# Kernel optimization log

Measured on AMD Instinct MI355X. Metric: run time of the kernel, lower is better.

## Reference

```python
import jax, jax.numpy as jnp
import numpy as np

N, F_IN, H, F_OUT, E = 50000, 128, 8, 16, 800000


def setup_inputs() -> dict:
    key = jax.random.key(0)
    ks = jax.random.split(key, 10)
    x = jax.random.normal(ks[0], (N, F_IN), dtype=jnp.float32)
    edge_index = jax.random.randint(ks[1], (2, E), 0, N, dtype=jnp.int64 if jax.config.read('jax_enable_x64') else jnp.int32)
    edge_prob = jax.random.uniform(ks[2], (E, 1), dtype=jnp.float32)
    s = 1.0 / np.sqrt(F_IN)
    Wp = jax.random.normal(ks[3], (H * F_OUT, F_IN), dtype=jnp.float32) * s
    Wt = jax.random.normal(ks[4], (H * F_OUT, 1), dtype=jnp.float32)
    a_src = jax.random.normal(ks[5], (H, F_OUT), dtype=jnp.float32) * 0.1
    a_trg = jax.random.normal(ks[6], (H, F_OUT), dtype=jnp.float32) * 0.1
    a_tp = jax.random.normal(ks[7], (H, F_OUT), dtype=jnp.float32) * 0.1
    Wskip = jax.random.normal(ks[8], (H * F_OUT, F_IN), dtype=jnp.float32) * s
    bias = jnp.zeros((H * F_OUT,), dtype=jnp.float32)
    return {"x": x, "edge_index": edge_index, "edge_prob": edge_prob,
            "Wp": Wp, "Wt": Wt, "a_src": a_src, "a_trg": a_trg,
            "a_tp": a_tp, "Wskip": Wskip, "bias": bias}


def reference(x, edge_index, edge_prob, Wp, Wt, a_src, a_trg, a_tp, Wskip, bias):
    n = x.shape[0]
    h, f = a_src.shape
    src, trg = edge_index[0], edge_index[1]
    # node projection: [N, H, F_out]
    proj = (x @ Wp.T).reshape(n, h, f)
    # transition-prob projection: [E, H, F_out]
    trans = (edge_prob @ Wt.T).reshape(-1, h, f)
    # per-node source/target scores [N, H], per-edge prob score [E, H]
    s_src = jnp.einsum('nhf,hf->nh', proj, a_src)
    s_trg = jnp.einsum('nhf,hf->nh', proj, a_trg)
    s_tp = jnp.einsum('ehf,hf->eh', trans, a_tp)
    scores = jax.nn.leaky_relu(s_src[src] + s_trg[trg] + s_tp, negative_slope=0.2)
    # global-max-shifted exp, segment softmax over target nodes
    e = jnp.exp(scores - jnp.max(scores))
    denom = jax.ops.segment_sum(e, trg, num_segments=n)
    attn = e / (denom[trg] + 1e-16)  # [E, H]
    weighted = proj[src] * attn[..., None]  # [E, H, F_out]
    out = jax.ops.segment_sum(weighted, trg, num_segments=n)  # [N, H, F_out]
    # skip connection (F_out != F_in -> skip_proj path), concat heads, bias, ELU
    out = out + (x @ Wskip.T).reshape(n, h, f)
    out = out.reshape(n, h * f) + bias
    return jax.nn.elu(out)
```

## Files before the change

### kernel.cpp

```cpp
#include <hip/hip_runtime.h>
#include <hip/hip_fp16.h>
#include <math.h>

constexpr int Nn  = 50000;
constexpr int FIN = 128;
constexpr int NH  = 8;
constexpr int FO  = 16;
constexpr int HF  = 128;
constexpr int NWR = 272;
constexpr int NPREP = NWR / 2;
constexpr int NBLK64 = (Nn + 63) / 64;
constexpr int NSCAN = (Nn + 255) / 256;

typedef _Float16 f16x8 __attribute__((ext_vector_type(8)));
typedef float    f32x4 __attribute__((ext_vector_type(4)));

__global__ __launch_bounds__(256) void k_pc(
    const float* __restrict__ Wp, const float* __restrict__ Wskip,
    const float* __restrict__ a_src, const float* __restrict__ a_trg,
    const float* __restrict__ Wt, const float* __restrict__ a_tp,
    _Float16* __restrict__ Wh, float* __restrict__ ctp,
    const int* __restrict__ trg, int* __restrict__ deg,
    int* __restrict__ rank, int E)
{
    const int bid = blockIdx.x;
    if (bid < NPREP) {
        if (bid == 0 && threadIdx.x < NH) {
            int h = threadIdx.x;
            float s = 0.f;
            #pragma unroll
            for (int f = 0; f < FO; ++f) s += Wt[h * FO + f] * a_tp[h * FO + f];
            ctp[h] = s;
        }
        const int o = bid * 2 + (threadIdx.x >> 7);
        const int k = threadIdx.x & 127;
        float v;
        if (o < 128)      v = Wp[o * FIN + k];
        else if (o < 256) v = Wskip[(o - 128) * FIN + k];
        else if (o < 264) {
            const int h = o - 256;
            float s = 0.f;
            #pragma unroll
            for (int f = 0; f < FO; ++f)
                s += a_src[h * FO + f] * Wp[(h * FO + f) * FIN + k];
            v = s;
        } else {
            const int h = o - 264;
            float s = 0.f;
            #pragma unroll
            for (int f = 0; f < FO; ++f)
                s += a_trg[h * FO + f] * Wp[(h * FO + f) * FIN + k];
            v = s;
        }
        Wh[o * FIN + k] = (_Float16)v;
        return;
    }

    int e = (bid - NPREP) * 256 + threadIdx.x;
    if (e < E) rank[e] = atomicAdd(&deg[trg[e]], 1);
}

__global__ __launch_bounds__(256) void k_scan1(const int* __restrict__ deg,
                                               int* __restrict__ partial)
{
    __shared__ int lds[256];
    int t = threadIdx.x, i = blockIdx.x * 256 + t;
    lds[t] = (i < Nn) ? deg[i] : 0;
    __syncthreads();
    for (int off = 128; off > 0; off >>= 1) {
        if (t < off) lds[t] += lds[t + off];
        __syncthreads();
    }
    if (t == 0) partial[blockIdx.x] = lds[0];
}

__global__ __launch_bounds__(256) void k_scan3(const int* __restrict__ deg,
                                               const int* __restrict__ partial,
                                               int* __restrict__ pos)
{
    __shared__ int lds[256], lds2[256];
    const int t = threadIdx.x;
    const int i = blockIdx.x * 256 + t;
    lds2[t] = (t < NSCAN) ? partial[t] : 0;
    __syncthreads();
    for (int off = 1; off < 256; off <<= 1) {
        int u = (t >= off) ? lds2[t - off] : 0;
        __syncthreads();
        lds2[t] += u;
        __syncthreads();
    }
    const int base = (blockIdx.x == 0) ? 0 : lds2[blockIdx.x - 1];
    int v = (i < Nn) ? deg[i] : 0;
    lds[t] = v;
    __syncthreads();
    for (int off = 1; off < 256; off <<= 1) {
        int u = (t >= off) ? lds[t - off] : 0;
        __syncthreads();
        lds[t] += u;
        __syncthreads();
    }
    if (i < Nn) pos[i] = base + lds[t] - v;
}

__global__ __launch_bounds__(256) void k_fn(
    const int* __restrict__ src, const int* __restrict__ trg,
    const float* __restrict__ prob, const int* __restrict__ rank,
    const int* __restrict__ pos, unsigned int* __restrict__ spk,
    const float* __restrict__ x, const _Float16* __restrict__ Wh,
    const float* __restrict__ bias,
    __half* __restrict__ projA, float* __restrict__ out,
    float* __restrict__ ssrc, float* __restrict__ strg_s, int E, int nbFill)
{
    const int bid = blockIdx.x;

    if (bid < nbFill) {
        int e4 = bid * 256 + threadIdx.x;
        if (e4 * 4 < E) {
            int4   s4 = reinterpret_cast<const int4*>(src)[e4];
            int4   t4 = reinterpret_cast<const int4*>(trg)[e4];
            float4 p4 = reinterpret_cast<const float4*>(prob)[e4];
            int4   r4 = reinterpret_cast<const int4*>(rank)[e4];
            int    sv[4] = {s4.x, s4.y, s4.z, s4.w};
            int    tv[4] = {t4.x, t4.y, t4.z, t4.w};
            int    rv[4] = {r4.x, r4.y, r4.z, r4.w};
            float  pv[4] = {p4.x, p4.y, p4.z, p4.w};
            #pragma unroll
            for (int i = 0; i < 4; ++i) {
                int slot = pos[tv[i]] + rv[i];
                spk[slot] = (unsigned int)sv[i] |
                    ((unsigned int)__half_as_ushort(__float2half_rn(pv[i])) << 16);
            }
        }
        return;
    }

    const int g0 = (bid - nbFill) * 64;
    const int w  = threadIdx.x >> 6;
    const int l  = threadIdx.x & 63;
    const int lr = l & 15;
    const int kb = l >> 4;
    const int t0 = w * 4;

    f16x8 b[4][4];
    const _Float16* wb = Wh + (size_t)lr * FIN + kb * 8;
    #pragma unroll
    for (int i = 0; i < 4; ++i) {
        #pragma unroll
        for (int ks = 0; ks < 4; ++ks)
            b[i][ks] = *reinterpret_cast<const f16x8*>(
                wb + (size_t)(t0 + i) * 16 * FIN + ks * 32);
    }
    f16x8 b16[4];
    if (w == 3) {
        #pragma unroll
        for (int ks = 0; ks < 4; ++ks)
            b16[ks] = *reinterpret_cast<const f16x8*>(
                wb + (size_t)16 * 16 * FIN + ks * 32);
    }

    const float* xr0 = x + (size_t)(g0 + lr) * FIN + kb * 8;

    if (g0 + 64 <= Nn) {
        float4 ucur[8];
        #pragma unroll
        for (int q = 0; q < 8; ++q)
            ucur[q] = *reinterpret_cast<const float4*>(
                xr0 + (q >> 1) * 32 + (q & 1) * 4);

        #pragma unroll
        for (int ng = 0; ng < 4; ++ng) {
            float4 unx[8];
            if (ng < 3) {
                const float* xrn = xr0 + (size_t)(ng + 1) * 16 * FIN;
                #pragma unroll
                for (int q = 0; q < 8; ++q)
                    unx[q] = *reinterpret_cast<const float4*>(
                        xrn + (q >> 1) * 32 + (q & 1) * 4);
            }

            f16x8 a[4];
            #pragma unroll
            for (int ks = 0; ks < 4; ++ks) {
                float4 lo = ucur[ks * 2], hi = ucur[ks * 2 + 1];
                a[ks][0] = (_Float16)lo.x; a[ks][1] = (_Float16)lo.y;
                a[ks][2] = (_Float16)lo.z; a[ks][3] = (_Float16)lo.w;
                a[ks][4] = (_Float16)hi.x; a[ks][5] = (_Float16)hi.y;
                a[ks][6] = (_Float16)hi.z; a[ks][7] = (_Float16)hi.w;
            }

            f32x4 acc[4];
            #pragma unroll
            for (int i = 0; i < 4; ++i) acc[i] = (f32x4){0.f, 0.f, 0.f, 0.f};
            f32x4 acc16 = (f32x4){0.f, 0.f, 0.f, 0.f};

            #pragma unroll
            for (int i = 0; i < 4; ++i) {
                #pragma unroll
                for (int ks = 0; ks < 4; ++ks)
                    acc[i] = __builtin_amdgcn_mfma_f32_16x16x32_f16(
                        a[ks], b[i][ks], acc[i], 0, 0, 0);
            }
            if (w == 3) {
                #pragma unroll
                for (int ks = 0; ks < 4; ++ks)
                    acc16 = __builtin_amdgcn_mfma_f32_16x16x32_f16(
                        a[ks], b16[ks], acc16, 0, 0, 0);
            }

            const int n0 = g0 + ng * 16;
            #pragma unroll
            for (int r = 0; r < 4; ++r) {
                const int n = n0 + kb * 4 + r;
                if (t0 < 8) {
                    #pragma unroll
                    for (int i = 0; i < 4; ++i)
                        projA[(size_t)n * HF + (t0 + i) * FO + lr] =
                            __float2half_rn(acc[i][r]);
                } else {
                    #pragma unroll
                    for (int i = 0; i < 4; ++i) {
                        const int o = (t0 + i - 8) * 16 + lr;
                        out[(size_t)n * HF + o] = acc[i][r] + bias[o];
                    }
                }
                if (w == 3) {
                    if (lr < 8) ssrc[n * 8 + lr] = acc16[r];
                    else        strg_s[n * 8 + (lr - 8)] = acc16[r];
                }
            }

            #pragma unroll
            for (int q = 0; q < 8; ++q) ucur[q] = unx[q];
        }
    } else {
        f16x8 a[4];
        #pragma unroll
        for (int ks = 0; ks < 4; ++ks) {
            float4 u0 = *reinterpret_cast<const float4*>(xr0 + ks * 32);
            float4 u1 = *reinterpret_cast<const float4*>(xr0 + ks * 32 + 4);
            a[ks][0] = (_Float16)u0.x; a[ks][1] = (_Float16)u0.y;
            a[ks][2] = (_Float16)u0.z; a[ks][3] = (_Float16)u0.w;
            a[ks][4] = (_Float16)u1.x; a[ks][5] = (_Float16)u1.y;
            a[ks][6] = (_Float16)u1.z; a[ks][7] = (_Float16)u1.w;
        }

        f32x4 acc[4];
        #pragma unroll
        for (int i = 0; i < 4; ++i) acc[i] = (f32x4){0.f, 0.f, 0.f, 0.f};
        f32x4 acc16 = (f32x4){0.f, 0.f, 0.f, 0.f};

        #pragma unroll
        for (int i = 0; i < 4; ++i) {
            #pragma unroll
            for (int ks = 0; ks < 4; ++ks)
                acc[i] = __builtin_amdgcn_mfma_f32_16x16x32_f16(
                    a[ks], b[i][ks], acc[i], 0, 0, 0);
        }
        if (w == 3) {
            #pragma unroll
            for (int ks = 0; ks < 4; ++ks)
                acc16 = __builtin_amdgcn_mfma_f32_16x16x32_f16(
                    a[ks], b16[ks], acc16, 0, 0, 0);
        }

        #pragma unroll
        for (int r = 0; r < 4; ++r) {
            const int n = g0 + kb * 4 + r;
            if (t0 < 8) {
                #pragma unroll
                for (int i = 0; i < 4; ++i)
                    projA[(size_t)n * HF + (t0 + i) * FO + lr] =
                        __float2half_rn(acc[i][r]);
            } else {
                #pragma unroll
                for (int i = 0; i < 4; ++i) {
                    const int o = (t0 + i - 8) * 16 + lr;
                    out[(size_t)n * HF + o] = acc[i][r] + bias[o];
                }
            }
            if (w == 3) {
                if (lr < 8) ssrc[n * 8 + lr] = acc16[r];
                else        strg_s[n * 8 + (lr - 8)] = acc16[r];
            }
        }
    }
}

__global__ __launch_bounds__(256) void k_gather(
    const unsigned int* __restrict__ spk, const int* __restrict__ pos,
    const float* __restrict__ ssrc, const float* __restrict__ strg_s,
    const float* __restrict__ ctp,
    const __half2* __restrict__ projA, float* __restrict__ out, int E)
{
    const int wv   = threadIdx.x >> 6;
    const int n    = blockIdx.x * 4 + wv;
    const int lane = threadIdx.x & 63;
    const int h    = lane >> 3;
    const int f2   = lane & 7;

    const int jb = pos[n];
    const int je = (n + 1 < Nn) ? pos[n + 1] : E;
    const float st  = strg_s[n * 8 + h];
    const float cth = ctp[h];
    const float* __restrict__ ssl = ssrc + h;
    const __half2* __restrict__ pA = projA + h * 8 + f2;

    float num0 = 0.f, num1 = 0.f, den = 0.f;
    int j = jb;
    for (; j + 3 < je; j += 4) {
        const unsigned int pk0 = spk[j];
        const unsigned int pk1 = spk[j + 1];
        const unsigned int pk2 = spk[j + 2];
        const unsigned int pk3 = spk[j + 3];
        const int s0 = pk0 & 0xFFFF, s1 = pk1 & 0xFFFF;
        const int s2 = pk2 & 0xFFFF, s3 = pk3 & 0xFFFF;
        const float ss0 = ssl[s0 * 8], ss1 = ssl[s1 * 8];
        const float ss2 = ssl[s2 * 8], ss3 = ssl[s3 * 8];
        const __half2 g0 = pA[s0 * 64], g1 = pA[s1 * 64];
        const __half2 g2 = pA[s2 * 64], g3 = pA[s3 * 64];
        const float p0 = __half2float(__ushort_as_half((unsigned short)(pk0 >> 16)));
        const float p1 = __half2float(__ushort_as_half((unsigned short)(pk1 >> 16)));
        const float p2 = __half2float(__ushort_as_half((unsigned short)(pk2 >> 16)));
        const float p3 = __half2float(__ushort_as_half((unsigned short)(pk3 >> 16)));
        float sc0 = ss0 + st + cth * p0;
        float sc1 = ss1 + st + cth * p1;
        float sc2 = ss2 + st + cth * p2;
        float sc3 = ss3 + st + cth * p3;
        sc0 = fmaxf(sc0, 0.2f * sc0);
        sc1 = fmaxf(sc1, 0.2f * sc1);
        sc2 = fmaxf(sc2, 0.2f * sc2);
        sc3 = fmaxf(sc3, 0.2f * sc3);
        const float ev0 = __expf(sc0), ev1 = __expf(sc1);
        const float ev2 = __expf(sc2), ev3 = __expf(sc3);
        const float2 G0 = __half22float2(g0), G1 = __half22float2(g1);
        const float2 G2 = __half22float2(g2), G3 = __half22float2(g3);
        den  += (ev0 + ev1) + (ev2 + ev3);
        num0 += ev0 * G0.x + ev1 * G1.x + ev2 * G2.x + ev3 * G3.x;
        num1 += ev0 * G0.y + ev1 * G1.y + ev2 * G2.y + ev3 * G3.y;
    }
    for (; j < je; ++j) {
        const unsigned int pk = spk[j];
        const int s = pk & 0xFFFF;
        const float p = __half2float(__ushort_as_half((unsigned short)(pk >> 16)));
        float sc = ssl[s * 8] + st + cth * p;
        sc = fmaxf(sc, 0.2f * sc);
        const float ev = __expf(sc);
        const float2 G = __half22float2(pA[s * 64]);
        den  += ev;
        num0 += ev * G.x;
        num1 += ev * G.y;
    }

    const float inv = 1.f / (den + 1e-16f);
    const int idx = n * HF + h * FO + f2 * 2;
    float2 o = *reinterpret_cast<const float2*>(&out[idx]);
    float v0 = o.x + num0 * inv;
    float v1 = o.y + num1 * inv;
    v0 = v0 > 0.f ? v0 : expm1f(v0);
    v1 = v1 > 0.f ? v1 : expm1f(v1);
    *reinterpret_cast<float2*>(&out[idx]) = make_float2(v0, v1);
}

extern "C" void kernel_launch(void* const* d_in, const int* in_sizes, int n_in,
                              void* d_out, int out_size, void* d_ws, size_t ws_size,
                              hipStream_t stream)
{
    const float* x     = (const float*)d_in[0];
    const int*   ei    = (const int*)d_in[1];
    const float* prob  = (const float*)d_in[2];
    const float* Wp    = (const float*)d_in[3];
    const float* Wt    = (const float*)d_in[4];
    const float* a_src = (const float*)d_in[5];
    const float* a_trg = (const float*)d_in[6];
    const float* a_tp  = (const float*)d_in[7];
    const float* Wskip = (const float*)d_in[8];
    const float* bias  = (const float*)d_in[9];
    float* out = (float*)d_out;

    const int E = in_sizes[2];
    const int* src = ei;
    const int* trg = ei + E;

    char* wsb = (char*)d_ws;
    __half* projA  = (__half*)wsb;
    float* ssrc    = (float*)(wsb + (size_t)Nn*HF*2);
    float* strg_s  = ssrc + (size_t)Nn * 8;
    float* ctp     = strg_s + (size_t)Nn * 8;
    _Float16* Wh   = (_Float16*)(ctp + 16);
    unsigned int* spk = (unsigned int*)(Wh + (size_t)NWR * FIN);
    int*   rank    = (int*)(spk + E);
    int*   deg     = rank + E;
    int*   pos     = deg + Nn;
    int*   partial = pos + Nn;

    const int nbCount = (E + 255) / 256;
    const int nbFill  = (E + 1023) / 1024;

    hipMemsetAsync(deg, 0, (size_t)Nn * sizeof(int), stream);
    k_pc<<<NPREP + nbCount, 256, 0, stream>>>(Wp, Wskip, a_src, a_trg, Wt,
                                              a_tp, Wh, ctp, trg, deg, rank, E);
    k_scan1<<<NSCAN, 256, 0, stream>>>(deg, partial);
    k_scan3<<<NSCAN, 256, 0, stream>>>(deg, partial, pos);
    k_fn<<<nbFill + NBLK64, 256, 0, stream>>>(src, trg, prob, rank, pos, spk,
                                              x, Wh, bias, projA, out,
                                              ssrc, strg_s, E, nbFill);
    k_gather<<<Nn / 4, 256, 0, stream>>>(spk, pos, ssrc, strg_s, ctp,
                                         (const __half2*)projA, out, E);
}
```

Baseline: 139.5 us.

## Split projection and scores into head-pair planes; gather per head-pair group

Result: slower. 179.9 us (+28.9%).

```diff
diff --git a/kernel.cpp b/kernel.cpp
--- a/kernel.cpp
+++ b/kernel.cpp
@@ -11,6 +11,8 @@
 constexpr int NPREP = NWR / 2;
 constexpr int NBLK64 = (Nn + 63) / 64;
 constexpr int NSCAN = (Nn + 255) / 256;
+constexpr int NPW = 10;
+constexpr int NGB = Nn / (NPW * 4);
 
 typedef _Float16 f16x8 __attribute__((ext_vector_type(8)));
 typedef float    f32x4 __attribute__((ext_vector_type(4)));
@@ -108,8 +110,8 @@
     const int* __restrict__ pos, unsigned int* __restrict__ spk,
     const float* __restrict__ x, const _Float16* __restrict__ Wh,
     const float* __restrict__ bias,
-    __half* __restrict__ projA, float* __restrict__ out,
-    float* __restrict__ ssrc, float* __restrict__ strg_s, int E, int nbFill)
+    __half* __restrict__ projG, float* __restrict__ out,
+    float* __restrict__ ssg, float* __restrict__ stg, int E, int nbFill)
 {
     const int bid = blockIdx.x;
 
@@ -213,9 +215,11 @@
                 const int n = n0 + kb * 4 + r;
                 if (t0 < 8) {
                     #pragma unroll
-                    for (int i = 0; i < 4; ++i)
-                        projA[(size_t)n * HF + (t0 + i) * FO + lr] =
-                            __float2half_rn(acc[i][r]);
+                    for (int i = 0; i < 4; ++i) {
+                        const int t = t0 + i;
+                        projG[(size_t)(t >> 1) * Nn * 32 + (size_t)n * 32 +
+                              (t & 1) * 16 + lr] = __float2half_rn(acc[i][r]);
+                    }
                 } else {
                     #pragma unroll
                     for (int i = 0; i < 4; ++i) {
@@ -224,8 +228,12 @@
                     }
                 }
                 if (w == 3) {
-                    if (lr < 8) ssrc[n * 8 + lr] = acc16[r];
-                    else        strg_s[n * 8 + (lr - 8)] = acc16[r];
+                    if (lr < 8)
+                        ssg[(size_t)(lr >> 1) * 2 * Nn + n * 2 + (lr & 1)] = acc16[r];
+                    else {
+                        const int hq = lr - 8;
+                        stg[(size_t)(hq >> 1) * 2 * Nn + n * 2 + (hq & 1)] = acc16[r];
+                    }
                 }
             }
 
@@ -268,9 +276,11 @@
             const int n = g0 + kb * 4 + r;
             if (t0 < 8) {
                 #pragma unroll
-                for (int i = 0; i < 4; ++i)
-                    projA[(size_t)n * HF + (t0 + i) * FO + lr] =
-                        __float2half_rn(acc[i][r]);
+                for (int i = 0; i < 4; ++i) {
+                    const int t = t0 + i;
+                    projG[(size_t)(t >> 1) * Nn * 32 + (size_t)n * 32 +
+                          (t & 1) * 16 + lr] = __float2half_rn(acc[i][r]);
+                }
             } else {
                 #pragma unroll
                 for (int i = 0; i < 4; ++i) {
@@ -279,8 +289,12 @@
                 }
             }
             if (w == 3) {
-                if (lr < 8) ssrc[n * 8 + lr] = acc16[r];
-                else        strg_s[n * 8 + (lr - 8)] = acc16[r];
+                if (lr < 8)
+                    ssg[(size_t)(lr >> 1) * 2 * Nn + n * 2 + (lr & 1)] = acc16[r];
+                else {
+                    const int hq = lr - 8;
+                    stg[(size_t)(hq >> 1) * 2 * Nn + n * 2 + (hq & 1)] = acc16[r];
+                }
             }
         }
     }
@@ -288,77 +302,89 @@
 
 __global__ __launch_bounds__(256) void k_gather(
     const unsigned int* __restrict__ spk, const int* __restrict__ pos,
-    const float* __restrict__ ssrc, const float* __restrict__ strg_s,
+    const float* __restrict__ ssg, const float* __restrict__ stg,
     const float* __restrict__ ctp,
-    const __half2* __restrict__ projA, float* __restrict__ out, int E)
-{
+    const __half2* __restrict__ projG2, float* __restrict__ out, int E)
+{
+    const int bid = blockIdx.x;
+    const int g   = bid & 3;
+    const int nb  = bid >> 2;
     const int wv   = threadIdx.x >> 6;
-    const int n    = blockIdx.x * 4 + wv;
     const int lane = threadIdx.x & 63;
-    const int h    = lane >> 3;
+    const int slot = lane >> 4;
+    const int hh   = (lane >> 3) & 1;
     const int f2   = lane & 7;
 
-    const int jb = pos[n];
-    const int je = (n + 1 < Nn) ? pos[n + 1] : E;
-    const float st  = strg_s[n * 8 + h];
-    const float cth = ctp[h];
-    const float* __restrict__ ssl = ssrc + h;
-    const __half2* __restrict__ pA = projA + h * 8 + f2;
-
-    float num0 = 0.f, num1 = 0.f, den = 0.f;
-    int j = jb;
-    for (; j + 3 < je; j += 4) {
-        const unsigned int pk0 = spk[j];
-        const unsigned int pk1 = spk[j + 1];
-        const unsigned int pk2 = spk[j + 2];
-        const unsigned int pk3 = spk[j + 3];
-        const int s0 = pk0 & 0xFFFF, s1 = pk1 & 0xFFFF;
-        const int s2 = pk2 & 0xFFFF, s3 = pk3 & 0xFFFF;
-        const float ss0 = ssl[s0 * 8], ss1 = ssl[s1 * 8];
-        const float ss2 = ssl[s2 * 8], ss3 = ssl[s3 * 8];
-        const __half2 g0 = pA[s0 * 64], g1 = pA[s1 * 64];
-        const __half2 g2 = pA[s2 * 64], g3 = pA[s3 * 64];
-        const float p0 = __half2float(__ushort_as_half((unsigned short)(pk0 >> 16)));
-        const float p1 = __half2float(__ushort_as_half((unsigned short)(pk1 >> 16)));
-        const float p2 = __half2float(__ushort_as_half((unsigned short)(pk2 >> 16)));
-        const float p3 = __half2float(__ushort_as_half((unsigned short)(pk3 >> 16)));
-        float sc0 = ss0 + st + cth * p0;
-        float sc1 = ss1 + st + cth * p1;
-        float sc2 = ss2 + st + cth * p2;
-        float sc3 = ss3 + st + cth * p3;
-        sc0 = fmaxf(sc0, 0.2f * sc0);
-        sc1 = fmaxf(sc1, 0.2f * sc1);
-        sc2 = fmaxf(sc2, 0.2f * sc2);
-        sc3 = fmaxf(sc3, 0.2f * sc3);
-        const float ev0 = __expf(sc0), ev1 = __expf(sc1);
-        const float ev2 = __expf(sc2), ev3 = __expf(sc3);
-        const float2 G0 = __half22float2(g0), G1 = __half22float2(g1);
-        const float2 G2 = __half22float2(g2), G3 = __half22float2(g3);
-        den  += (ev0 + ev1) + (ev2 + ev3);
-        num0 += ev0 * G0.x + ev1 * G1.x + ev2 * G2.x + ev3 * G3.x;
-        num1 += ev0 * G0.y + ev1 * G1.y + ev2 * G2.y + ev3 * G3.y;
-    }
-    for (; j < je; ++j) {
-        const unsigned int pk = spk[j];
-        const int s = pk & 0xFFFF;
-        const float p = __half2float(__ushort_as_half((unsigned short)(pk >> 16)));
-        float sc = ssl[s * 8] + st + cth * p;
-        sc = fmaxf(sc, 0.2f * sc);
-        const float ev = __expf(sc);
-        const float2 G = __half22float2(pA[s * 64]);
-        den  += ev;
-        num0 += ev * G.x;
-        num1 += ev * G.y;
-    }
-
-    const float inv = 1.f / (den + 1e-16f);
-    const int idx = n * HF + h * FO + f2 * 2;
-    float2 o = *reinterpret_cast<const float2*>(&out[idx]);
-    float v0 = o.x + num0 * inv;
-    float v1 = o.y + num1 * inv;
-    v0 = v0 > 0.f ? v0 : expm1f(v0);
-    v1 = v1 > 0.f ? v1 : expm1f(v1);
-    *reinterpret_cast<float2*>(&out[idx]) = make_float2(v0, v1);
+    const float cth = ctp[g * 2 + hh];
+    const float* __restrict__ ssl = ssg + (size_t)g * 2 * Nn + hh;
+    const float* __restrict__ stl = stg + (size_t)g * 2 * Nn + hh;
+    const __half2* __restrict__ pG = projG2 + (size_t)g * Nn * 16 + hh * 8 + f2;
+
+    const int nbase = (nb * 4 + wv) * NPW;
+
+    for (int nn = 0; nn < NPW; ++nn) {
+        const int n = nbase + nn;
+        const int jb = pos[n];
+        const int je = (n + 1 < Nn) ? pos[n + 1] : E;
+        const float st = stl[n * 2];
+
+        float num0 = 0.f, num1 = 0.f, den = 0.f;
+        int j = jb + slot;
+        for (; j + 4 < je; j += 8) {
+            const unsigned int pk0 = spk[j];
+            const unsigned int pk1 = spk[j + 4];
+            const int s0 = pk0 & 0xFFFF;
+            const int s1 = pk1 & 0xFFFF;
+            const float ss0 = ssl[s0 * 2];
+            const float ss1 = ssl[s1 * 2];
+            const __half2 g0 = pG[s0 * 16];
+            const __half2 g1 = pG[s1 * 16];
+            const float p0 = __half2float(__ushort_as_half((unsigned short)(pk0 >> 16)));
+            const float p1 = __half2float(__ushort_as_half((unsigned short)(pk1 >> 16)));
+            float sc0 = ss0 + st + cth * p0;
+            float sc1 = ss1 + st + cth * p1;
+            sc0 = fmaxf(sc0, 0.2f * sc0);
+            sc1 = fmaxf(sc1, 0.2f * sc1);
+            const float ev0 = __expf(sc0);
+            const float ev1 = __expf(sc1);
+            const float2 G0 = __half22float2(g0);
+            const float2 G1 = __half22float2(g1);
+            den  += ev0 + ev1;
+            num0 += ev0 * G0.x + ev1 * G1.x;
+            num1 += ev0 * G0.y + ev1 * G1.y;
+        }
+        if (j < je) {
+            const unsigned int pk = spk[j];
+            const int s = pk & 0xFFFF;
+            const float p = __half2float(__ushort_as_half((unsigned short)(pk >> 16)));
+            float sc = ssl[s * 2] + st + cth * p;
+            sc = fmaxf(sc, 0.2f * sc);
+            const float ev = __expf(sc);
+            const float2 G = __half22float2(pG[s * 16]);
+            den  += ev;
+            num0 += ev * G.x;
+            num1 += ev * G.y;
+        }
+
+        num0 += __shfl_xor(num0, 16, 64);
+        num1 += __shfl_xor(num1, 16, 64);
+        den  += __shfl_xor(den,  16, 64);
+        num0 += __shfl_xor(num0, 32, 64);
+        num1 += __shfl_xor(num1, 32, 64);
+        den  += __shfl_xor(den,  32, 64);
+
+        if (slot == 0) {
+            const int h = g * 2 + hh;
+            const int idx = n * HF + h * FO + f2 * 2;
+            const float inv = 1.f / (den + 1e-16f);
+            float2 o = *reinterpret_cast<const float2*>(&out[idx]);
+            float v0 = o.x + num0 * inv;
+            float v1 = o.y + num1 * inv;
+            v0 = v0 > 0.f ? v0 : expm1f(v0);
+            v1 = v1 > 0.f ? v1 : expm1f(v1);
+            *reinterpret_cast<float2*>(&out[idx]) = make_float2(v0, v1);
+        }
+    }
 }
 
 extern "C" void kernel_launch(void* const* d_in, const int* in_sizes, int n_in,
@@ -382,10 +408,10 @@
     const int* trg = ei + E;
 
     char* wsb = (char*)d_ws;
-    __half* projA  = (__half*)wsb;
-    float* ssrc    = (float*)(wsb + (size_t)Nn*HF*2);
-    float* strg_s  = ssrc + (size_t)Nn * 8;
-    float* ctp     = strg_s + (size_t)Nn * 8;
+    __half* projG  = (__half*)wsb;
+    float* ssg     = (float*)(wsb + (size_t)Nn*HF*2);
+    float* stg     = ssg + (size_t)4 * Nn * 2;
+    float* ctp     = stg + (size_t)4 * Nn * 2;
     _Float16* Wh   = (_Float16*)(ctp + 16);
     unsigned int* spk = (unsigned int*)(Wh + (size_t)NWR * FIN);
     int*   rank    = (int*)(spk + E);
@@ -402,8 +428,8 @@
     k_scan1<<<NSCAN, 256, 0, stream>>>(deg, partial);
     k_scan3<<<NSCAN, 256, 0, stream>>>(deg, partial, pos);
     k_fn<<<nbFill + NBLK64, 256, 0, stream>>>(src, trg, prob, rank, pos, spk,
-                                              x, Wh, bias, projA, out,
-                                              ssrc, strg_s, E, nbFill);
-    k_gather<<<Nn / 4, 256, 0, stream>>>(spk, pos, ssrc, strg_s, ctp,
-                                         (const __half2*)projA, out, E);
-}
+                                              x, Wh, bias, projG, out,
+                                              ssg, stg, E, nbFill);
+    k_gather<<<4 * NGB, 256, 0, stream>>>(spk, pos, ssg, stg, ctp,
+                                          (const __half2*)projG, out, E);
+}
```
